# Kernel tuning notes

Measured on AMD Instinct MI355X. Metric: run time of the kernel, lower is better.

Reference implementation:

```python
import jax, jax.numpy as jnp
import numpy as np

BOOST_STRENGTH = 1.0  # init kwarg boostStrength (already >= 0)


def setup_inputs() -> dict:
    key = jax.random.key(0)
    k1, k2 = jax.random.split(key)
    x = jax.random.normal(k1, (8192, 4096), dtype=jnp.float32)
    # duty cycles are running fractions of activity, roughly around k/n
    dutyCycles = jax.random.uniform(k2, (4096,), dtype=jnp.float32) * 0.2
    return {"x": x, "dutyCycles": dutyCycles, "k": 409}


def reference(x, dutyCycles, k):
    n = x.shape[1]
    boost_strength = jnp.maximum(jnp.float32(BOOST_STRENGTH), 0.0)
    target_density = jnp.float32(k) / jnp.float32(n)
    # boostFactors = exp[(targetDensity - dutyCycle) * boostStrength]
    boost_factors = jnp.exp((target_density - dutyCycles) * boost_strength)  # [n]
    boosted = x * boost_factors  # [B, n]
    topk_vals, _ = jax.lax.top_k(boosted, k)  # [B, k]
    bottom = jnp.min(topk_vals, axis=1, keepdims=True)  # per-row k-th largest
    mask = (boosted >= bottom).astype(x.dtype)
    return x * mask
```

## Files before the change

### kernel.cpp

```cpp
#include <hip/hip_runtime.h>
#include <cstdint>
#include <cstddef>

#define N_COLS 4096
#define TPB 256
#define NCOPY 8
#define HSTR 12
#define NHWORDS (256 * HSTR)
#define SURV_CAP 64

__global__ void boost_kernel(const float* __restrict__ dc,
                             const int* __restrict__ kp,
                             float* __restrict__ bf) {
    int i = blockIdx.x * blockDim.x + threadIdx.x;
    if (i < N_COLS) {
        float td = (float)kp[0] / (float)N_COLS;
        float arg = td - dc[i];
        bf[i] = (float)exp((double)arg);
    }
}

__device__ __forceinline__ uint32_t orderable(uint32_t u) {
    return (u & 0x80000000u) ? ~u : (u | 0x80000000u);
}

__global__ __launch_bounds__(TPB) void kwinner_kernel(
    const float* __restrict__ x, const float* __restrict__ bf,
    const int* __restrict__ kp, float* __restrict__ out)
{
    __shared__ uint32_t s_hist[NHWORDS];
    __shared__ uint32_t s_cnt[256];
    __shared__ uint32_t s_cand[SURV_CAP];
    __shared__ uint32_t s_m2;

    const int tid  = threadIdx.x;
    const int lane = tid & 63;
    const uint32_t copy = (uint32_t)(tid & (NCOPY - 1));
    const size_t row = blockIdx.x;
    const float4* xr = (const float4*)(x + row * (size_t)N_COLS);
    const float4* br = (const float4*)bf;
    float4* orow = (float4*)(out + row * (size_t)N_COLS);

    float4 xv[4];
    float xb[16];
    #pragma unroll
    for (int j = 0; j < 4; ++j) {
        float4 v = xr[tid + j * TPB];
        float4 b = br[tid + j * TPB];
        xv[j] = v;
        xb[j * 4 + 0] = v.x * b.x;
        xb[j * 4 + 1] = v.y * b.y;
        xb[j * 4 + 2] = v.z * b.z;
        xb[j * 4 + 3] = v.w * b.w;
    }

    {
        uint4* h4 = (uint4*)s_hist;
        uint4 z; z.x = z.y = z.z = z.w = 0u;
        #pragma unroll
        for (int j = 0; j < 3; ++j) h4[tid + j * TPB] = z;
    }
    if (tid == 0) s_m2 = 0;
    __syncthreads();

    const float T0f = 1.10f;
    #pragma unroll
    for (int e = 0; e < 16; ++e) {
        if (xb[e] >= T0f) {
            uint32_t d = (__float_as_uint(xb[e]) >> 16) - 0x3F80u;
            d = d > 255u ? 255u : d;
            atomicAdd(&s_hist[d * HSTR + copy], 1u);
        }
    }
    __syncthreads();

    const uint32_t k = (uint32_t)kp[0];
    uint32_t rem = k;

    uint32_t dsel;
    uint32_t packed;
    {
        uint32_t vv[4];
        const uint32_t b0 = (uint32_t)lane * 4u;
        #pragma unroll
        for (int i = 0; i < 4; ++i) {
            uint4 a  = *(const uint4*)&s_hist[(b0 + i) * HSTR];
            uint4 b2 = *(const uint4*)&s_hist[(b0 + i) * HSTR + 4];
            vv[i] = a.x + a.y + a.z + a.w + b2.x + b2.y + b2.z + b2.w;
        }
        uint32_t s3 = vv[3], s2 = vv[2] + s3, s1 = vv[1] + s2, s0 = vv[0] + s1;
        uint32_t T = s0;
        #pragma unroll
        for (int off = 1; off < 64; off <<= 1) {
            uint32_t t = (uint32_t)__shfl_down((int)T, off, 64);
            if (lane + off < 64) T += t;
        }
        uint32_t Tex = T - s0;
        uint32_t S0 = Tex + s0, S1 = Tex + s1, S2 = Tex + s2, S3 = Tex + s3;
        int b = -1; uint32_t sn = 0;
        if (S3 >= rem)      { b = 3; sn = S3 - vv[3]; }
        else if (S2 >= rem) { b = 2; sn = S2 - vv[2]; }
        else if (S1 >= rem) { b = 1; sn = S1 - vv[1]; }
        else if (S0 >= rem) { b = 0; sn = S0 - vv[0]; }
        packed = (b >= 0) ? ((((uint32_t)(4 * lane + b + 1)) << 16) | sn) : 0u;
        #pragma unroll
        for (int off = 1; off < 64; off <<= 1) {
            uint32_t o = (uint32_t)__shfl_xor((int)packed, off, 64);
            packed = packed > o ? packed : o;
        }
        dsel = (packed >> 16) - 1u;
        rem -= (packed & 0xFFFFu);
    }

    float thr = 0.0f;
    bool need_fallback = (packed == 0u) || (dsel == 255u);

    if (!need_fallback) {
        const uint32_t hi16 = 0x3F80u + dsel;
        #pragma unroll
        for (int e = 0; e < 16; ++e) {
            uint32_t ub = __float_as_uint(xb[e]);
            if ((ub >> 16) == hi16) {
                uint32_t pos = atomicAdd(&s_m2, 1u);
                if (pos < SURV_CAP) s_cand[pos] = ub;
            }
        }
        __syncthreads();
        const uint32_t m2 = s_m2;
        if (m2 <= SURV_CAP) {
            uint32_t cv = ((uint32_t)lane < m2) ? s_cand[lane] : ((~hi16) << 16);
            uint32_t cur = 0;
            #pragma unroll
            for (int bpos = 15; bpos >= 0; --bpos) {
                uint32_t t  = (hi16 << 16) | cur | (1u << bpos);
                uint32_t mk = ~((1u << bpos) - 1u);
                uint32_t c  = (uint32_t)__popcll(__ballot(((cv ^ t) & mk) == 0u));
                if (c >= rem) cur |= (1u << bpos);
                else          rem -= c;
            }
            thr = __uint_as_float((hi16 << 16) | cur);
        } else {
            need_fallback = true;
        }
    }

    if (need_fallback) {
        __syncthreads();
        {
            uint4* h4 = (uint4*)s_hist;
            uint4 z; z.x = z.y = z.z = z.w = 0u;
            #pragma unroll
            for (int j = 0; j < 3; ++j) h4[tid + j * TPB] = z;
        }
        __syncthreads();
        uint32_t prefix = 0;
        rem = k;
        const uint32_t pmasks[4] = {0u, 0xFF000000u, 0xFFFF0000u, 0xFFFFFF00u};
        #pragma unroll 1
        for (int pass = 0; pass < 4; ++pass) {
            const int shift = 24 - pass * 8;
            const uint32_t pm = pmasks[pass];
            #pragma unroll
            for (int e = 0; e < 16; ++e) {
                uint32_t ou = orderable(__float_as_uint(xb[e]));
                if (((ou ^ prefix) & pm) == 0u)
                    atomicAdd(&s_hist[((ou >> shift) & 255u) * HSTR + copy], 1u);
            }
            __syncthreads();
            {
                uint4 a  = *(const uint4*)&s_hist[tid * HSTR];
                uint4 b2 = *(const uint4*)&s_hist[tid * HSTR + 4];
                uint4 z; z.x = z.y = z.z = z.w = 0u;
                *(uint4*)&s_hist[tid * HSTR]     = z;
                *(uint4*)&s_hist[tid * HSTR + 4] = z;
                s_cnt[tid] = a.x + a.y + a.z + a.w + b2.x + b2.y + b2.z + b2.w;
            }
            __syncthreads();
            uint4 v = ((const uint4*)s_cnt)[lane];
            uint32_t s3 = v.w, s2 = v.z + s3, s1 = v.y + s2, s0 = v.x + s1;
            uint32_t T = s0;
            #pragma unroll
            for (int off = 1; off < 64; off <<= 1) {
                uint32_t t = (uint32_t)__shfl_down((int)T, off, 64);
                if (lane + off < 64) T += t;
            }
            uint32_t Tex = T - s0;
            uint32_t S0 = Tex + s0, S1 = Tex + s1, S2 = Tex + s2, S3 = Tex + s3;
            int b = -1; uint32_t sn = 0;
            if (S3 >= rem)      { b = 3; sn = S3 - v.w; }
            else if (S2 >= rem) { b = 2; sn = S2 - v.z; }
            else if (S1 >= rem) { b = 1; sn = S1 - v.y; }
            else if (S0 >= rem) { b = 0; sn = S0 - v.x; }
            uint32_t pk = (b >= 0) ? ((((uint32_t)(4 * lane + b + 1)) << 16) | sn) : 0u;
            #pragma unroll
            for (int off = 1; off < 64; off <<= 1) {
                uint32_t o = (uint32_t)__shfl_xor((int)pk, off, 64);
                pk = pk > o ? pk : o;
            }
            prefix |= ((pk >> 16) - 1u) << shift;
            rem -= (pk & 0xFFFFu);
        }
        uint32_t tu = (prefix & 0x80000000u) ? (prefix & 0x7FFFFFFFu) : ~prefix;
        thr = __uint_as_float(tu);
    }

    #pragma unroll
    for (int j = 0; j < 4; ++j) {
        float4 o;
        o.x = (xb[j * 4 + 0] >= thr) ? xv[j].x : 0.0f;
        o.y = (xb[j * 4 + 1] >= thr) ? xv[j].y : 0.0f;
        o.z = (xb[j * 4 + 2] >= thr) ? xv[j].z : 0.0f;
        o.w = (xb[j * 4 + 3] >= thr) ? xv[j].w : 0.0f;
        orow[tid + j * TPB] = o;
    }
}

extern "C" void kernel_launch(void* const* d_in, const int* in_sizes, int n_in,
                              void* d_out, int out_size, void* d_ws, size_t ws_size,
                              hipStream_t stream) {
    const float* x  = (const float*)d_in[0];
    const float* dc = (const float*)d_in[1];
    const int*   kp = (const int*)d_in[2];
    float* out = (float*)d_out;
    float* bf  = (float*)d_ws;

    const int n    = in_sizes[1];
    const int rows = in_sizes[0] / n;

    boost_kernel<<<(n + TPB - 1) / TPB, TPB, 0, stream>>>(dc, kp, bf);
    kwinner_kernel<<<rows, TPB, 0, stream>>>(x, bf, kp, out);
}
```

Before: 230.6 us.

## Process two rows per block with interleaved histograms and nontemporal stores

Each block now handles two rows at once, interleaving their histogram builds, scans, candidate collection and bit descents to raise instruction-level parallelism and halve the block count. Raw x values are no longer kept in registers; they are reloaded from global memory for the masked output. Output uses nontemporal stores. The cost is higher register pressure and shared memory per block, plus the extra re-read of x through cache, all of which may lower occupancy.

```diff
diff --git a/kernel.cpp b/kernel.cpp
--- a/kernel.cpp
+++ b/kernel.cpp
@@ -6,8 +6,14 @@
 #define TPB 256
 #define NCOPY 8
 #define HSTR 12
-#define NHWORDS (256 * HSTR)
+#define NHW (256 * HSTR)
 #define SURV_CAP 64
+
+typedef float v4f __attribute__((ext_vector_type(4)));
+
+__device__ __forceinline__ void store_nt(float4* p, const float4& v) {
+    __builtin_nontemporal_store(*(const v4f*)&v, (v4f*)p);
+}
 
 __global__ void boost_kernel(const float* __restrict__ dc,
                              const int* __restrict__ kp,
@@ -26,66 +32,71 @@
 
 __global__ __launch_bounds__(TPB) void kwinner_kernel(
     const float* __restrict__ x, const float* __restrict__ bf,
-    const int* __restrict__ kp, float* __restrict__ out)
+    const int* __restrict__ kp, float* __restrict__ out, int rows)
 {
-    __shared__ uint32_t s_hist[NHWORDS];
+    __shared__ uint32_t s_hist[2 * NHW];
     __shared__ uint32_t s_cnt[256];
-    __shared__ uint32_t s_cand[SURV_CAP];
-    __shared__ uint32_t s_m2;
+    __shared__ uint32_t s_cand[2][SURV_CAP];
+    __shared__ uint32_t s_m2[2];
 
     const int tid  = threadIdx.x;
     const int lane = tid & 63;
     const uint32_t copy = (uint32_t)(tid & (NCOPY - 1));
-    const size_t row = blockIdx.x;
-    const float4* xr = (const float4*)(x + row * (size_t)N_COLS);
-    const float4* br = (const float4*)bf;
-    float4* orow = (float4*)(out + row * (size_t)N_COLS);
-
-    float4 xv[4];
-    float xb[16];
+    const int rowA = 2 * (int)blockIdx.x;
+    const int rowB = rowA + 1;
+    const bool validB = rowB < rows;
+    const float4* xrA = (const float4*)(x + (size_t)rowA * N_COLS);
+    const float4* xrB = (const float4*)(x + (size_t)(validB ? rowB : rowA) * N_COLS);
+    const float4* br  = (const float4*)bf;
+    float4* orowA = (float4*)(out + (size_t)rowA * N_COLS);
+    float4* orowB = (float4*)(out + (size_t)rowB * N_COLS);
+
+    float xbA[16], xbB[16];
     #pragma unroll
     for (int j = 0; j < 4; ++j) {
-        float4 v = xr[tid + j * TPB];
         float4 b = br[tid + j * TPB];
-        xv[j] = v;
-        xb[j * 4 + 0] = v.x * b.x;
-        xb[j * 4 + 1] = v.y * b.y;
-        xb[j * 4 + 2] = v.z * b.z;
-        xb[j * 4 + 3] = v.w * b.w;
+        float4 a = xrA[tid + j * TPB];
+        float4 c = xrB[tid + j * TPB];
+        xbA[4*j+0] = a.x*b.x; xbA[4*j+1] = a.y*b.y;
+        xbA[4*j+2] = a.z*b.z; xbA[4*j+3] = a.w*b.w;
+        xbB[4*j+0] = c.x*b.x; xbB[4*j+1] = c.y*b.y;
+        xbB[4*j+2] = c.z*b.z; xbB[4*j+3] = c.w*b.w;
     }
 
     {
         uint4* h4 = (uint4*)s_hist;
         uint4 z; z.x = z.y = z.z = z.w = 0u;
         #pragma unroll
-        for (int j = 0; j < 3; ++j) h4[tid + j * TPB] = z;
-    }
-    if (tid == 0) s_m2 = 0;
+        for (int j = 0; j < 6; ++j) h4[tid + j * TPB] = z;
+    }
+    if (tid < 2) s_m2[tid] = 0;
     __syncthreads();
 
     const float T0f = 1.10f;
     #pragma unroll
     for (int e = 0; e < 16; ++e) {
-        if (xb[e] >= T0f) {
-            uint32_t d = (__float_as_uint(xb[e]) >> 16) - 0x3F80u;
+        if (xbA[e] >= T0f) {
+            uint32_t d = (__float_as_uint(xbA[e]) >> 16) - 0x3F80u;
             d = d > 255u ? 255u : d;
             atomicAdd(&s_hist[d * HSTR + copy], 1u);
         }
+        if (xbB[e] >= T0f) {
+            uint32_t d = (__float_as_uint(xbB[e]) >> 16) - 0x3F80u;
+            d = d > 255u ? 255u : d;
+            atomicAdd(&s_hist[NHW + d * HSTR + copy], 1u);
+        }
     }
     __syncthreads();
 
     const uint32_t k = (uint32_t)kp[0];
-    uint32_t rem = k;
-
-    uint32_t dsel;
-    uint32_t packed;
-    {
+
+    auto scan_row = [&](const uint32_t* hist, uint32_t& remr) -> uint32_t {
         uint32_t vv[4];
         const uint32_t b0 = (uint32_t)lane * 4u;
         #pragma unroll
         for (int i = 0; i < 4; ++i) {
-            uint4 a  = *(const uint4*)&s_hist[(b0 + i) * HSTR];
-            uint4 b2 = *(const uint4*)&s_hist[(b0 + i) * HSTR + 4];
+            uint4 a  = *(const uint4*)&hist[(b0 + i) * HSTR];
+            uint4 b2 = *(const uint4*)&hist[(b0 + i) * HSTR + 4];
             vv[i] = a.x + a.y + a.z + a.w + b2.x + b2.y + b2.z + b2.w;
         }
         uint32_t s3 = vv[3], s2 = vv[2] + s3, s1 = vv[1] + s2, s0 = vv[0] + s1;
@@ -98,53 +109,67 @@
         uint32_t Tex = T - s0;
         uint32_t S0 = Tex + s0, S1 = Tex + s1, S2 = Tex + s2, S3 = Tex + s3;
         int b = -1; uint32_t sn = 0;
-        if (S3 >= rem)      { b = 3; sn = S3 - vv[3]; }
-        else if (S2 >= rem) { b = 2; sn = S2 - vv[2]; }
-        else if (S1 >= rem) { b = 1; sn = S1 - vv[1]; }
-        else if (S0 >= rem) { b = 0; sn = S0 - vv[0]; }
-        packed = (b >= 0) ? ((((uint32_t)(4 * lane + b + 1)) << 16) | sn) : 0u;
+        if (S3 >= remr)      { b = 3; sn = S3 - vv[3]; }
+        else if (S2 >= remr) { b = 2; sn = S2 - vv[2]; }
+        else if (S1 >= remr) { b = 1; sn = S1 - vv[1]; }
+        else if (S0 >= remr) { b = 0; sn = S0 - vv[0]; }
+        uint32_t pk = (b >= 0) ? ((((uint32_t)(4 * lane + b + 1)) << 16) | sn) : 0u;
         #pragma unroll
         for (int off = 1; off < 64; off <<= 1) {
-            uint32_t o = (uint32_t)__shfl_xor((int)packed, off, 64);
-            packed = packed > o ? packed : o;
-        }
-        dsel = (packed >> 16) - 1u;
-        rem -= (packed & 0xFFFFu);
-    }
-
-    float thr = 0.0f;
-    bool need_fallback = (packed == 0u) || (dsel == 255u);
-
-    if (!need_fallback) {
-        const uint32_t hi16 = 0x3F80u + dsel;
-        #pragma unroll
-        for (int e = 0; e < 16; ++e) {
-            uint32_t ub = __float_as_uint(xb[e]);
-            if ((ub >> 16) == hi16) {
-                uint32_t pos = atomicAdd(&s_m2, 1u);
-                if (pos < SURV_CAP) s_cand[pos] = ub;
-            }
-        }
-        __syncthreads();
-        const uint32_t m2 = s_m2;
-        if (m2 <= SURV_CAP) {
-            uint32_t cv = ((uint32_t)lane < m2) ? s_cand[lane] : ((~hi16) << 16);
-            uint32_t cur = 0;
-            #pragma unroll
-            for (int bpos = 15; bpos >= 0; --bpos) {
-                uint32_t t  = (hi16 << 16) | cur | (1u << bpos);
-                uint32_t mk = ~((1u << bpos) - 1u);
-                uint32_t c  = (uint32_t)__popcll(__ballot(((cv ^ t) & mk) == 0u));
-                if (c >= rem) cur |= (1u << bpos);
-                else          rem -= c;
-            }
-            thr = __uint_as_float((hi16 << 16) | cur);
-        } else {
-            need_fallback = true;
-        }
-    }
-
-    if (need_fallback) {
+            uint32_t o = (uint32_t)__shfl_xor((int)pk, off, 64);
+            pk = pk > o ? pk : o;
+        }
+        remr -= (pk & 0xFFFFu);
+        return pk;
+    };
+
+    uint32_t remA = k, remB = k;
+    const uint32_t pkA = scan_row(s_hist, remA);
+    const uint32_t pkB = scan_row(s_hist + NHW, remB);
+    const uint32_t dselA = (pkA >> 16) - 1u;
+    const uint32_t dselB = (pkB >> 16) - 1u;
+    bool fbA = (pkA == 0u) || (dselA == 255u);
+    bool fbB = (pkB == 0u) || (dselB == 255u);
+    const uint32_t hiA = 0x3F80u + dselA;
+    const uint32_t hiB = 0x3F80u + dselB;
+
+    #pragma unroll
+    for (int e = 0; e < 16; ++e) {
+        uint32_t ua = __float_as_uint(xbA[e]);
+        if (!fbA && (ua >> 16) == hiA) {
+            uint32_t pos = atomicAdd(&s_m2[0], 1u);
+            if (pos < SURV_CAP) s_cand[0][pos] = ua;
+        }
+        uint32_t ub = __float_as_uint(xbB[e]);
+        if (!fbB && (ub >> 16) == hiB) {
+            uint32_t pos = atomicAdd(&s_m2[1], 1u);
+            if (pos < SURV_CAP) s_cand[1][pos] = ub;
+        }
+    }
+    __syncthreads();
+    const uint32_t m2A = s_m2[0];
+    const uint32_t m2B = s_m2[1];
+
+    auto descent = [&](uint32_t hi16, const uint32_t* cand, uint32_t m2,
+                       uint32_t rem) -> float {
+        uint32_t cv = ((uint32_t)lane < m2) ? cand[lane] : ((~hi16) << 16);
+        uint32_t cur = 0;
+        #pragma unroll
+        for (int bpos = 15; bpos >= 0; --bpos) {
+            uint32_t t  = (hi16 << 16) | cur | (1u << bpos);
+            uint32_t mk = ~((1u << bpos) - 1u);
+            uint32_t c  = (uint32_t)__popcll(__ballot(((cv ^ t) & mk) == 0u));
+            if (c >= rem) cur |= (1u << bpos);
+            else          rem -= c;
+        }
+        return __uint_as_float((hi16 << 16) | cur);
+    };
+
+    float thrA = 0.0f, thrB = 0.0f;
+    if (!fbA) { if (m2A <= SURV_CAP) thrA = descent(hiA, s_cand[0], m2A, remA); else fbA = true; }
+    if (!fbB) { if (m2B <= SURV_CAP) thrB = descent(hiB, s_cand[1], m2B, remB); else fbB = true; }
+
+    auto fallback_row = [&](const float* xb) -> float {
         __syncthreads();
         {
             uint4* h4 = (uint4*)s_hist;
@@ -153,8 +178,7 @@
             for (int j = 0; j < 3; ++j) h4[tid + j * TPB] = z;
         }
         __syncthreads();
-        uint32_t prefix = 0;
-        rem = k;
+        uint32_t prefix = 0, rem = k;
         const uint32_t pmasks[4] = {0u, 0xFF000000u, 0xFFFF0000u, 0xFFFFFF00u};
         #pragma unroll 1
         for (int pass = 0; pass < 4; ++pass) {
@@ -201,17 +225,33 @@
             rem -= (pk & 0xFFFFu);
         }
         uint32_t tu = (prefix & 0x80000000u) ? (prefix & 0x7FFFFFFFu) : ~prefix;
-        thr = __uint_as_float(tu);
-    }
+        return __uint_as_float(tu);
+    };
+
+    if (fbA) thrA = fallback_row(xbA);
+    if (fbB) thrB = fallback_row(xbB);
 
     #pragma unroll
     for (int j = 0; j < 4; ++j) {
+        float4 a = xrA[tid + j * TPB];
         float4 o;
-        o.x = (xb[j * 4 + 0] >= thr) ? xv[j].x : 0.0f;
-        o.y = (xb[j * 4 + 1] >= thr) ? xv[j].y : 0.0f;
-        o.z = (xb[j * 4 + 2] >= thr) ? xv[j].z : 0.0f;
-        o.w = (xb[j * 4 + 3] >= thr) ? xv[j].w : 0.0f;
-        orow[tid + j * TPB] = o;
+        o.x = (xbA[4*j+0] >= thrA) ? a.x : 0.0f;
+        o.y = (xbA[4*j+1] >= thrA) ? a.y : 0.0f;
+        o.z = (xbA[4*j+2] >= thrA) ? a.z : 0.0f;
+        o.w = (xbA[4*j+3] >= thrA) ? a.w : 0.0f;
+        store_nt(&orowA[tid + j * TPB], o);
+    }
+    if (validB) {
+        #pragma unroll
+        for (int j = 0; j < 4; ++j) {
+            float4 c = xrB[tid + j * TPB];
+            float4 o;
+            o.x = (xbB[4*j+0] >= thrB) ? c.x : 0.0f;
+            o.y = (xbB[4*j+1] >= thrB) ? c.y : 0.0f;
+            o.z = (xbB[4*j+2] >= thrB) ? c.z : 0.0f;
+            o.w = (xbB[4*j+3] >= thrB) ? c.w : 0.0f;
+            store_nt(&orowB[tid + j * TPB], o);
+        }
     }
 }
 
@@ -228,5 +268,5 @@
     const int rows = in_sizes[0] / n;
 
     boost_kernel<<<(n + TPB - 1) / TPB, TPB, 0, stream>>>(dc, kp, bf);
-    kwinner_kernel<<<rows, TPB, 0, stream>>>(x, bf, kp, out);
-}
+    kwinner_kernel<<<(rows + 1) / 2, TPB, 0, stream>>>(x, bf, kp, out, rows);
+}
```

After: 238.0 us. +3.2%, slower.

## Process one row per wavefront with re-read from cache instead of registers

Applied to the files above, without the earlier changes.

Restructures the k-winner kernel so each 64-lane wavefront handles a whole row, with a private shared histogram, and replaces block-wide barriers with wavefront-local fences. Rows are re-read from global memory (expected to hit cache) in each pass instead of being held in registers, and outputs use nontemporal stores. Launch bounds request higher occupancy. The aim is to remove __syncthreads and multi-copy histogram reduction overhead, at the cost of extra global reads per row and more atomic contention on a single histogram copy.

```diff
diff --git a/kernel.cpp b/kernel.cpp
--- a/kernel.cpp
+++ b/kernel.cpp
@@ -4,10 +4,14 @@
 
 #define N_COLS 4096
 #define TPB 256
-#define NCOPY 8
-#define HSTR 12
-#define NHWORDS (256 * HSTR)
+#define WPB 4
+#define NBINS 256
 #define SURV_CAP 64
+
+typedef float v4f __attribute__((ext_vector_type(4)));
+__device__ __forceinline__ void store_nt(float4* p, const float4& v) {
+    __builtin_nontemporal_store(*(const v4f*)&v, (v4f*)p);
+}
 
 __global__ void boost_kernel(const float* __restrict__ dc,
                              const int* __restrict__ kp,
@@ -24,71 +28,54 @@
     return (u & 0x80000000u) ? ~u : (u | 0x80000000u);
 }
 
-__global__ __launch_bounds__(TPB) void kwinner_kernel(
+__global__ __launch_bounds__(TPB, 6) void kwinner_kernel(
     const float* __restrict__ x, const float* __restrict__ bf,
-    const int* __restrict__ kp, float* __restrict__ out)
+    const int* __restrict__ kp, float* __restrict__ out, int rows)
 {
-    __shared__ uint32_t s_hist[NHWORDS];
-    __shared__ uint32_t s_cnt[256];
-    __shared__ uint32_t s_cand[SURV_CAP];
-    __shared__ uint32_t s_m2;
+    __shared__ uint32_t s_hist[WPB][NBINS];
+    __shared__ uint32_t s_cand[WPB][SURV_CAP];
+    __shared__ uint32_t s_m2[WPB];
 
     const int tid  = threadIdx.x;
+    const int wid  = tid >> 6;
     const int lane = tid & 63;
-    const uint32_t copy = (uint32_t)(tid & (NCOPY - 1));
-    const size_t row = blockIdx.x;
-    const float4* xr = (const float4*)(x + row * (size_t)N_COLS);
+    const int row  = (int)blockIdx.x * WPB + wid;
+    if (row >= rows) return;
+
+    uint32_t* hist = s_hist[wid];
+    uint32_t* cand = s_cand[wid];
+    const float4* xr = (const float4*)(x + (size_t)row * N_COLS);
     const float4* br = (const float4*)bf;
-    float4* orow = (float4*)(out + row * (size_t)N_COLS);
-
-    float4 xv[4];
-    float xb[16];
-    #pragma unroll
-    for (int j = 0; j < 4; ++j) {
-        float4 v = xr[tid + j * TPB];
-        float4 b = br[tid + j * TPB];
-        xv[j] = v;
-        xb[j * 4 + 0] = v.x * b.x;
-        xb[j * 4 + 1] = v.y * b.y;
-        xb[j * 4 + 2] = v.z * b.z;
-        xb[j * 4 + 3] = v.w * b.w;
-    }
-
-    {
-        uint4* h4 = (uint4*)s_hist;
-        uint4 z; z.x = z.y = z.z = z.w = 0u;
+    float4* orow = (float4*)(out + (size_t)row * N_COLS);
+
+    { uint4 z; z.x = z.y = z.z = z.w = 0u; ((uint4*)hist)[lane] = z; }
+    if (lane == 0) s_m2[wid] = 0;
+    __threadfence_block();
+
+    const float T0f = 1.10f;
+    #pragma unroll 4
+    for (int j = 0; j < 16; ++j) {
+        float4 a = xr[lane + j * 64];
+        float4 b = br[lane + j * 64];
+        float p[4] = {a.x * b.x, a.y * b.y, a.z * b.z, a.w * b.w};
         #pragma unroll
-        for (int j = 0; j < 3; ++j) h4[tid + j * TPB] = z;
-    }
-    if (tid == 0) s_m2 = 0;
-    __syncthreads();
-
-    const float T0f = 1.10f;
-    #pragma unroll
-    for (int e = 0; e < 16; ++e) {
-        if (xb[e] >= T0f) {
-            uint32_t d = (__float_as_uint(xb[e]) >> 16) - 0x3F80u;
-            d = d > 255u ? 255u : d;
-            atomicAdd(&s_hist[d * HSTR + copy], 1u);
-        }
-    }
-    __syncthreads();
+        for (int q = 0; q < 4; ++q) {
+            if (p[q] >= T0f) {
+                uint32_t d = (__float_as_uint(p[q]) >> 16) - 0x3F80u;
+                d = d > 255u ? 255u : d;
+                atomicAdd(&hist[d], 1u);
+            }
+        }
+    }
+    __threadfence_block();
 
     const uint32_t k = (uint32_t)kp[0];
     uint32_t rem = k;
 
-    uint32_t dsel;
-    uint32_t packed;
+    uint32_t pk;
     {
-        uint32_t vv[4];
-        const uint32_t b0 = (uint32_t)lane * 4u;
-        #pragma unroll
-        for (int i = 0; i < 4; ++i) {
-            uint4 a  = *(const uint4*)&s_hist[(b0 + i) * HSTR];
-            uint4 b2 = *(const uint4*)&s_hist[(b0 + i) * HSTR + 4];
-            vv[i] = a.x + a.y + a.z + a.w + b2.x + b2.y + b2.z + b2.w;
-        }
-        uint32_t s3 = vv[3], s2 = vv[2] + s3, s1 = vv[1] + s2, s0 = vv[0] + s1;
+        uint4 v = ((const uint4*)hist)[lane];
+        uint32_t s3 = v.w, s2 = v.z + s3, s1 = v.y + s2, s0 = v.x + s1;
         uint32_t T = s0;
         #pragma unroll
         for (int off = 1; off < 64; off <<= 1) {
@@ -98,37 +85,42 @@
         uint32_t Tex = T - s0;
         uint32_t S0 = Tex + s0, S1 = Tex + s1, S2 = Tex + s2, S3 = Tex + s3;
         int b = -1; uint32_t sn = 0;
-        if (S3 >= rem)      { b = 3; sn = S3 - vv[3]; }
-        else if (S2 >= rem) { b = 2; sn = S2 - vv[2]; }
-        else if (S1 >= rem) { b = 1; sn = S1 - vv[1]; }
-        else if (S0 >= rem) { b = 0; sn = S0 - vv[0]; }
-        packed = (b >= 0) ? ((((uint32_t)(4 * lane + b + 1)) << 16) | sn) : 0u;
+        if (S3 >= rem)      { b = 3; sn = S3 - v.w; }
+        else if (S2 >= rem) { b = 2; sn = S2 - v.z; }
+        else if (S1 >= rem) { b = 1; sn = S1 - v.y; }
+        else if (S0 >= rem) { b = 0; sn = S0 - v.x; }
+        pk = (b >= 0) ? ((((uint32_t)(4 * lane + b + 1)) << 16) | sn) : 0u;
         #pragma unroll
         for (int off = 1; off < 64; off <<= 1) {
-            uint32_t o = (uint32_t)__shfl_xor((int)packed, off, 64);
-            packed = packed > o ? packed : o;
-        }
-        dsel = (packed >> 16) - 1u;
-        rem -= (packed & 0xFFFFu);
-    }
-
+            uint32_t o = (uint32_t)__shfl_xor((int)pk, off, 64);
+            pk = pk > o ? pk : o;
+        }
+        rem -= (pk & 0xFFFFu);
+    }
+    const uint32_t dsel = (pk >> 16) - 1u;
+    bool fb = (pk == 0u) || (dsel == 255u);
     float thr = 0.0f;
-    bool need_fallback = (packed == 0u) || (dsel == 255u);
-
-    if (!need_fallback) {
+
+    if (!fb) {
         const uint32_t hi16 = 0x3F80u + dsel;
-        #pragma unroll
-        for (int e = 0; e < 16; ++e) {
-            uint32_t ub = __float_as_uint(xb[e]);
-            if ((ub >> 16) == hi16) {
-                uint32_t pos = atomicAdd(&s_m2, 1u);
-                if (pos < SURV_CAP) s_cand[pos] = ub;
-            }
-        }
-        __syncthreads();
-        const uint32_t m2 = s_m2;
+        #pragma unroll 4
+        for (int j = 0; j < 16; ++j) {
+            float4 a = xr[lane + j * 64];
+            float4 b = br[lane + j * 64];
+            float p[4] = {a.x * b.x, a.y * b.y, a.z * b.z, a.w * b.w};
+            #pragma unroll
+            for (int q = 0; q < 4; ++q) {
+                uint32_t ub = __float_as_uint(p[q]);
+                if ((ub >> 16) == hi16) {
+                    uint32_t pos = atomicAdd(&s_m2[wid], 1u);
+                    if (pos < SURV_CAP) cand[pos] = ub;
+                }
+            }
+        }
+        __threadfence_block();
+        const uint32_t m2 = s_m2[wid];
         if (m2 <= SURV_CAP) {
-            uint32_t cv = ((uint32_t)lane < m2) ? s_cand[lane] : ((~hi16) << 16);
+            uint32_t cv = ((uint32_t)lane < m2) ? cand[lane] : ((~hi16) << 16);
             uint32_t cur = 0;
             #pragma unroll
             for (int bpos = 15; bpos >= 0; --bpos) {
@@ -140,43 +132,34 @@
             }
             thr = __uint_as_float((hi16 << 16) | cur);
         } else {
-            need_fallback = true;
-        }
-    }
-
-    if (need_fallback) {
-        __syncthreads();
-        {
-            uint4* h4 = (uint4*)s_hist;
-            uint4 z; z.x = z.y = z.z = z.w = 0u;
-            #pragma unroll
-            for (int j = 0; j < 3; ++j) h4[tid + j * TPB] = z;
-        }
-        __syncthreads();
+            fb = true;
+        }
+    }
+
+    if (fb) {
         uint32_t prefix = 0;
         rem = k;
         const uint32_t pmasks[4] = {0u, 0xFF000000u, 0xFFFF0000u, 0xFFFFFF00u};
         #pragma unroll 1
         for (int pass = 0; pass < 4; ++pass) {
+            { uint4 z; z.x = z.y = z.z = z.w = 0u; ((uint4*)hist)[lane] = z; }
+            __threadfence_block();
             const int shift = 24 - pass * 8;
             const uint32_t pm = pmasks[pass];
-            #pragma unroll
-            for (int e = 0; e < 16; ++e) {
-                uint32_t ou = orderable(__float_as_uint(xb[e]));
-                if (((ou ^ prefix) & pm) == 0u)
-                    atomicAdd(&s_hist[((ou >> shift) & 255u) * HSTR + copy], 1u);
-            }
-            __syncthreads();
-            {
-                uint4 a  = *(const uint4*)&s_hist[tid * HSTR];
-                uint4 b2 = *(const uint4*)&s_hist[tid * HSTR + 4];
-                uint4 z; z.x = z.y = z.z = z.w = 0u;
-                *(uint4*)&s_hist[tid * HSTR]     = z;
-                *(uint4*)&s_hist[tid * HSTR + 4] = z;
-                s_cnt[tid] = a.x + a.y + a.z + a.w + b2.x + b2.y + b2.z + b2.w;
-            }
-            __syncthreads();
-            uint4 v = ((const uint4*)s_cnt)[lane];
+            #pragma unroll 2
+            for (int j = 0; j < 16; ++j) {
+                float4 a = xr[lane + j * 64];
+                float4 b = br[lane + j * 64];
+                float p[4] = {a.x * b.x, a.y * b.y, a.z * b.z, a.w * b.w};
+                #pragma unroll
+                for (int q = 0; q < 4; ++q) {
+                    uint32_t ou = orderable(__float_as_uint(p[q]));
+                    if (((ou ^ prefix) & pm) == 0u)
+                        atomicAdd(&hist[(ou >> shift) & 255u], 1u);
+                }
+            }
+            __threadfence_block();
+            uint4 v = ((const uint4*)hist)[lane];
             uint32_t s3 = v.w, s2 = v.z + s3, s1 = v.y + s2, s0 = v.x + s1;
             uint32_t T = s0;
             #pragma unroll
@@ -191,27 +174,30 @@
             else if (S2 >= rem) { b = 2; sn = S2 - v.z; }
             else if (S1 >= rem) { b = 1; sn = S1 - v.y; }
             else if (S0 >= rem) { b = 0; sn = S0 - v.x; }
-            uint32_t pk = (b >= 0) ? ((((uint32_t)(4 * lane + b + 1)) << 16) | sn) : 0u;
+            uint32_t pk2 = (b >= 0) ? ((((uint32_t)(4 * lane + b + 1)) << 16) | sn) : 0u;
             #pragma unroll
             for (int off = 1; off < 64; off <<= 1) {
-                uint32_t o = (uint32_t)__shfl_xor((int)pk, off, 64);
-                pk = pk > o ? pk : o;
-            }
-            prefix |= ((pk >> 16) - 1u) << shift;
-            rem -= (pk & 0xFFFFu);
+                uint32_t o = (uint32_t)__shfl_xor((int)pk2, off, 64);
+                pk2 = pk2 > o ? pk2 : o;
+            }
+            prefix |= ((pk2 >> 16) - 1u) << shift;
+            rem -= (pk2 & 0xFFFFu);
+            __threadfence_block();
         }
         uint32_t tu = (prefix & 0x80000000u) ? (prefix & 0x7FFFFFFFu) : ~prefix;
         thr = __uint_as_float(tu);
     }
 
-    #pragma unroll
-    for (int j = 0; j < 4; ++j) {
+    #pragma unroll 4
+    for (int j = 0; j < 16; ++j) {
+        float4 a = xr[lane + j * 64];
+        float4 b = br[lane + j * 64];
         float4 o;
-        o.x = (xb[j * 4 + 0] >= thr) ? xv[j].x : 0.0f;
-        o.y = (xb[j * 4 + 1] >= thr) ? xv[j].y : 0.0f;
-        o.z = (xb[j * 4 + 2] >= thr) ? xv[j].z : 0.0f;
-        o.w = (xb[j * 4 + 3] >= thr) ? xv[j].w : 0.0f;
-        orow[tid + j * TPB] = o;
+        o.x = (a.x * b.x >= thr) ? a.x : 0.0f;
+        o.y = (a.y * b.y >= thr) ? a.y : 0.0f;
+        o.z = (a.z * b.z >= thr) ? a.z : 0.0f;
+        o.w = (a.w * b.w >= thr) ? a.w : 0.0f;
+        store_nt(&orow[lane + j * 64], o);
     }
 }
 
@@ -228,5 +214,5 @@
     const int rows = in_sizes[0] / n;
 
     boost_kernel<<<(n + TPB - 1) / TPB, TPB, 0, stream>>>(dc, kp, bf);
-    kwinner_kernel<<<rows, TPB, 0, stream>>>(x, bf, kp, out);
-}
+    kwinner_kernel<<<(rows + WPB - 1) / WPB, TPB, 0, stream>>>(x, bf, kp, out, rows);
+}
```

After: 267.4 us. 1.16x slower.
